# Kernel tuning notes

Hardware: AMD Instinct MI355X
Metric: run time of the kernel (lower is better)

## Reference

```python
import jax, jax.numpy as jnp
import numpy as np

BOUND = 10.0
EPS = 1e-06
MIN_SCALE = 1e-4


def _params_to_spline(raw_w, raw_h, raw_s, bound):
    # Standard Durkan et al. rational-quadratic spline parameterization.
    # raw_w/raw_h: (1, D, K); raw_s: (1, D, K+1)
    two_b = 2.0 * bound
    widths = jax.nn.softmax(raw_w[0], axis=-1) * two_b      # (D, K)
    heights = jax.nn.softmax(raw_h[0], axis=-1) * two_b     # (D, K)
    zero = jnp.zeros(widths.shape[:-1] + (1,), widths.dtype)
    xk = -bound + jnp.concatenate([zero, jnp.cumsum(widths, axis=-1)], axis=-1)   # (D, K+1)
    yk = -bound + jnp.concatenate([zero, jnp.cumsum(heights, axis=-1)], axis=-1)  # (D, K+1)
    slopes = jax.nn.softplus(raw_s[0])                       # (D, K+1)
    return xk, yk, widths, heights, slopes


def _rqs_forward(z, xk, yk, widths, heights, slopes, bound):
    # z: (B, D); per-dim knots xk/yk: (D, K+1); widths/heights: (D, K); slopes: (D, K+1)
    B, D = z.shape
    K = widths.shape[-1]
    zc = jnp.clip(z, -bound, bound)
    # per-dim binary search over knot positions
    idx = jax.vmap(lambda knots, col: jnp.searchsorted(knots, col, side='right'),
                   in_axes=(0, 1), out_axes=1)(xk, zc) - 1
    idx = jnp.clip(idx, 0, K - 1)                            # (B, D)
    di = jnp.arange(D)[None, :]
    xk_sel = xk[di, idx]
    w_sel = widths[di, idx]
    yk_sel = yk[di, idx]
    h_sel = heights[di, idx]
    d0 = slopes[di, idx]
    d1 = slopes[di, idx + 1]
    theta = (zc - xk_sel) / w_sel
    s = h_sel / w_sel
    t1m = theta * (1.0 - theta)
    den = s + (d0 + d1 - 2.0 * s) * t1m
    y_in = yk_sel + h_sel * (s * theta * theta + d0 * t1m) / den
    inside = (z > -bound) & (z < bound)
    return jnp.where(inside, y_in, z)


def setup_inputs() -> dict:
    key = jax.random.key(0)
    ks = jax.random.split(key, 7)
    B, D, K = 8192, 1024, 64
    return {
        'u': jax.random.uniform(ks[0], (B, D), dtype=jnp.float32),
        'tau': jax.random.normal(ks[1], (B, 1), dtype=jnp.float32),
        'log_scale': jax.random.normal(ks[2], (D,), dtype=jnp.float32) * 0.1,
        'bias': jax.random.normal(ks[3], (D,), dtype=jnp.float32) * 0.1,
        'raw_w': jax.random.normal(ks[4], (1, D, K), dtype=jnp.float32) * 0.5,
        'raw_h': jax.random.normal(ks[5], (1, D, K), dtype=jnp.float32) * 0.5,
        'raw_s': jax.random.normal(ks[6], (1, D, K + 1), dtype=jnp.float32) * 0.5,
    }


def reference(u, tau, log_scale, bias, raw_w, raw_h, raw_s):
    # logit input transform
    u_safe = jnp.clip(u, EPS, 1.0 - EPS)
    z = jnp.log(u_safe) - jnp.log1p(-u_safe)
    xk, yk, widths, heights, slopes = _params_to_spline(raw_w, raw_h, raw_s, BOUND)
    z = _rqs_forward(z, xk, yk, widths, heights, slopes, BOUND)
    scale = jax.nn.softplus(log_scale) + MIN_SCALE
    q = z * scale[None, :] + bias[None, :]
    return tau * q  # tau (B,1) broadcasts to (B,D)
```

## Files before the change

### kernel.cpp

```cpp
#include <hip/hip_runtime.h>
#include <math.h>

#define BOUNDF 10.0f
#define EPSF 1e-6f
#define MIN_SCALEF 1e-4f
#define DD 1024
#define KK 64
#define KP1 65

#define TD 64
#define TR 128

__global__ __launch_bounds__(64) void rqs_precompute(
    const float* __restrict__ raw_w, const float* __restrict__ raw_h,
    const float* __restrict__ raw_s, const float* __restrict__ log_scale,
    float* __restrict__ xk, float* __restrict__ yk,
    float* __restrict__ sl, float* __restrict__ scale)
{
    const int d = blockIdx.x;
    const int k = threadIdx.x;

    float ew = __expf(raw_w[d * KK + k]);
    float eh = __expf(raw_h[d * KK + k]);

    float sw = ew, sh = eh;
#pragma unroll
    for (int off = 1; off < 64; off <<= 1) {
        sw += __shfl_xor(sw, off, 64);
        sh += __shfl_xor(sh, off, 64);
    }
    float wk = ew * (2.0f * BOUNDF) / sw;
    float hk = eh * (2.0f * BOUNDF) / sh;

    float cw = wk, ch = hk;
#pragma unroll
    for (int off = 1; off < 64; off <<= 1) {
        float tw = __shfl_up(cw, off, 64);
        float th = __shfl_up(ch, off, 64);
        if (k >= off) { cw += tw; ch += th; }
    }
    xk[d * KP1 + k + 1] = -BOUNDF + cw;
    yk[d * KP1 + k + 1] = -BOUNDF + ch;

    float rs = raw_s[d * KP1 + k];
    sl[d * KP1 + k] = log1pf(__expf(rs));
    if (k == 0) {
        xk[d * KP1] = -BOUNDF;
        yk[d * KP1] = -BOUNDF;
        float rs2 = raw_s[d * KP1 + KK];
        sl[d * KP1 + KK] = log1pf(__expf(rs2));
        scale[d] = log1pf(__expf(log_scale[d])) + MIN_SCALEF;
    }
}

__global__ __launch_bounds__(256) void rqs_main(
    const float* __restrict__ u, const float* __restrict__ tau,
    const float* __restrict__ bias,
    const float* __restrict__ xk_g, const float* __restrict__ yk_g,
    const float* __restrict__ sl_g, const float* __restrict__ scale_g,
    float* __restrict__ out)
{
    __shared__ float lxk[TD * KP1];
    __shared__ float lyk[TD * KP1];
    __shared__ float lsl[TD * KP1];

    const int bx = blockIdx.x;
    const int dchunk = bx & (DD / TD - 1);
    const int rchunk = bx >> 4;
    const int d0 = dchunk * TD;
    const int r0 = rchunk * TR;
    const int t = threadIdx.x;

    for (int i = t; i < TD * KP1; i += 256) {
        lxk[i] = xk_g[d0 * KP1 + i];
        lyk[i] = yk_g[d0 * KP1 + i];
        lsl[i] = sl_g[d0 * KP1 + i];
    }
    __syncthreads();

    const int g = t & 15;
    const int rlane = t >> 4;
    const int dl = g * 4;
    const int dg = d0 + dl;

    float sc[4], bi[4];
#pragma unroll
    for (int j = 0; j < 4; ++j) {
        sc[j] = scale_g[dg + j];
        bi[j] = bias[dg + j];
    }

#pragma unroll 1
    for (int it = 0; it < TR / 16; ++it) {
        const int b = r0 + it * 16 + rlane;
        const float4 uu = *(const float4*)(u + (size_t)b * DD + dg);
        const float tb = tau[b];
        float ua[4] = {uu.x, uu.y, uu.z, uu.w};
        float res[4];
#pragma unroll
        for (int j = 0; j < 4; ++j) {
            float uv = fminf(fmaxf(ua[j], EPSF), 1.0f - EPSF);
            float z = __logf(uv) - __logf(1.0f - uv);
            float zc = fminf(fmaxf(z, -BOUNDF), BOUNDF);
            const int base = (dl + j) * KP1;
            int lo = 0;
#pragma unroll
            for (int s = 32; s >= 1; s >>= 1) {
                lo += (lxk[base + lo + s] <= zc) ? s : 0;
            }
            float x0 = lxk[base + lo], x1 = lxk[base + lo + 1];
            float y0 = lyk[base + lo], y1 = lyk[base + lo + 1];
            float s0 = lsl[base + lo], s1 = lsl[base + lo + 1];
            float w = x1 - x0, h = y1 - y0;
            float invw = __builtin_amdgcn_rcpf(w);
            float th = (zc - x0) * invw;
            float sm = h * invw;
            float t1m = th * (1.0f - th);
            float den = fmaf(fmaf(-2.0f, sm, s0 + s1), t1m, sm);
            float num = h * fmaf(sm * th, th, s0 * t1m);
            float y = fmaf(num, __builtin_amdgcn_rcpf(den), y0);
            y = (z > -BOUNDF && z < BOUNDF) ? y : z;
            res[j] = tb * fmaf(y, sc[j], bi[j]);
        }
        float4 ro = make_float4(res[0], res[1], res[2], res[3]);
        *(float4*)(out + (size_t)b * DD + dg) = ro;
    }
}

extern "C" void kernel_launch(void* const* d_in, const int* in_sizes, int n_in,
                              void* d_out, int out_size, void* d_ws, size_t ws_size,
                              hipStream_t stream)
{
    const float* u         = (const float*)d_in[0];
    const float* tau       = (const float*)d_in[1];
    const float* log_scale = (const float*)d_in[2];
    const float* bias      = (const float*)d_in[3];
    const float* raw_w     = (const float*)d_in[4];
    const float* raw_h     = (const float*)d_in[5];
    const float* raw_s     = (const float*)d_in[6];
    float* out = (float*)d_out;

    float* ws    = (float*)d_ws;
    float* xk    = ws;
    float* yk    = xk + DD * KP1;
    float* sl    = yk + DD * KP1;
    float* scale = sl + DD * KP1;

    const int B = in_sizes[0] / DD;

    rqs_precompute<<<DD, 64, 0, stream>>>(raw_w, raw_h, raw_s, log_scale,
                                          xk, yk, sl, scale);
    rqs_main<<<(DD / TD) * (B / TR), 256, 0, stream>>>(u, tau, bias,
                                                       xk, yk, sl, scale, out);
}
```

Measured before the change: 116.8 us.

## Halve D-tile, cache upper search knots in registers, prefetch next row

Shrinks the per-block D tile from 64 to 32, which halves the shared memory used for knot tables and allows more resident blocks; launch bounds now request 6 blocks. The first three levels of the per-element binary search now read from seven knot values held in registers instead of shared memory. The next row's u and tau are loaded before computing the current row, and the logit uses one log plus a reciprocal instead of two logs. In exchange, knot tables are reloaded from global memory by twice as many blocks, and the extra registers may pressure occupancy.

```diff
diff --git a/kernel.cpp b/kernel.cpp
--- a/kernel.cpp
+++ b/kernel.cpp
@@ -8,7 +8,7 @@
 #define KK 64
 #define KP1 65
 
-#define TD 64
+#define TD 32
 #define TR 128
 
 __global__ __launch_bounds__(64) void rqs_precompute(
@@ -53,7 +53,7 @@
     }
 }
 
-__global__ __launch_bounds__(256) void rqs_main(
+__global__ __launch_bounds__(256, 6) void rqs_main(
     const float* __restrict__ u, const float* __restrict__ tau,
     const float* __restrict__ bias,
     const float* __restrict__ xk_g, const float* __restrict__ yk_g,
@@ -66,7 +66,7 @@
 
     const int bx = blockIdx.x;
     const int dchunk = bx & (DD / TD - 1);
-    const int rchunk = bx >> 4;
+    const int rchunk = bx >> 5;
     const int d0 = dchunk * TD;
     const int r0 = rchunk * TR;
     const int t = threadIdx.x;
@@ -78,36 +78,55 @@
     }
     __syncthreads();
 
-    const int g = t & 15;
-    const int rlane = t >> 4;
+    const int g = t & 7;
+    const int rlane = t >> 3;
     const int dl = g * 4;
     const int dg = d0 + dl;
 
     float sc[4], bi[4];
+    float kreg[4][7];
 #pragma unroll
     for (int j = 0; j < 4; ++j) {
         sc[j] = scale_g[dg + j];
         bi[j] = bias[dg + j];
+        const int base = (dl + j) * KP1;
+#pragma unroll
+        for (int i = 0; i < 7; ++i) kreg[j][i] = lxk[base + 8 * (i + 1)];
     }
 
+    int b = r0 + rlane;
+    float4 uu = *(const float4*)(u + (size_t)b * DD + dg);
+    float tb = tau[b];
+
 #pragma unroll 1
-    for (int it = 0; it < TR / 16; ++it) {
-        const int b = r0 + it * 16 + rlane;
-        const float4 uu = *(const float4*)(u + (size_t)b * DD + dg);
-        const float tb = tau[b];
-        float ua[4] = {uu.x, uu.y, uu.z, uu.w};
+    for (int it = 0; it < TR / 32; ++it) {
+        const int bcur = b;
+        const float4 ucur = uu;
+        const float tcur = tb;
+        if (it + 1 < TR / 32) {
+            const int bn = bcur + 32;
+            uu = *(const float4*)(u + (size_t)bn * DD + dg);
+            tb = tau[bn];
+            b = bn;
+        }
+        float ua[4] = {ucur.x, ucur.y, ucur.z, ucur.w};
         float res[4];
 #pragma unroll
         for (int j = 0; j < 4; ++j) {
             float uv = fminf(fmaxf(ua[j], EPSF), 1.0f - EPSF);
-            float z = __logf(uv) - __logf(1.0f - uv);
+            float z = __logf(uv * __builtin_amdgcn_rcpf(1.0f - uv));
             float zc = fminf(fmaxf(z, -BOUNDF), BOUNDF);
             const int base = (dl + j) * KP1;
-            int lo = 0;
-#pragma unroll
-            for (int s = 32; s >= 1; s >>= 1) {
-                lo += (lxk[base + lo + s] <= zc) ? s : 0;
-            }
+            int lo = (zc >= kreg[j][3]) ? 32 : 0;
+            float m16 = (lo & 32) ? kreg[j][5] : kreg[j][1];
+            lo += (zc >= m16) ? 16 : 0;
+            float a8 = (lo & 32) ? kreg[j][4] : kreg[j][0];
+            float b8 = (lo & 32) ? kreg[j][6] : kreg[j][2];
+            float m8 = (lo & 16) ? b8 : a8;
+            lo += (zc >= m8) ? 8 : 0;
+            lo += (lxk[base + lo + 4] <= zc) ? 4 : 0;
+            lo += (lxk[base + lo + 2] <= zc) ? 2 : 0;
+            lo += (lxk[base + lo + 1] <= zc) ? 1 : 0;
             float x0 = lxk[base + lo], x1 = lxk[base + lo + 1];
             float y0 = lyk[base + lo], y1 = lyk[base + lo + 1];
             float s0 = lsl[base + lo], s1 = lsl[base + lo + 1];
@@ -120,10 +139,10 @@
             float num = h * fmaf(sm * th, th, s0 * t1m);
             float y = fmaf(num, __builtin_amdgcn_rcpf(den), y0);
             y = (z > -BOUNDF && z < BOUNDF) ? y : z;
-            res[j] = tb * fmaf(y, sc[j], bi[j]);
+            res[j] = tcur * fmaf(y, sc[j], bi[j]);
         }
         float4 ro = make_float4(res[0], res[1], res[2], res[3]);
-        *(float4*)(out + (size_t)b * DD + dg) = ro;
+        *(float4*)(out + (size_t)bcur * DD + dg) = ro;
     }
 }
 
```

Result: faster. 111.0 us (-5.0%).

## Map one thread per dimension and track search bounds in registers

Applied to the files above, without the earlier changes.

Shrinks the dimension tile from 64 to 32 and gives each thread a single dimension with scalar loads instead of float4 over four dimensions. This spreads shared-memory knot lookups across banks and avoids the strided-bank conflicts of the old mapping. The binary search now carries the bracketing knot values in registers, removing two shared loads, and the logit is computed with one log and a reciprocal. Softplus in the precompute kernel uses fast log. Costs are narrower 4-byte global accesses, more blocks each reloading the knot tables, and slightly lower precision in the logit and softplus.

```diff
diff --git a/kernel.cpp b/kernel.cpp
--- a/kernel.cpp
+++ b/kernel.cpp
@@ -8,7 +8,7 @@
 #define KK 64
 #define KP1 65
 
-#define TD 64
+#define TD 32
 #define TR 128
 
 __global__ __launch_bounds__(64) void rqs_precompute(
@@ -43,13 +43,13 @@
     yk[d * KP1 + k + 1] = -BOUNDF + ch;
 
     float rs = raw_s[d * KP1 + k];
-    sl[d * KP1 + k] = log1pf(__expf(rs));
+    sl[d * KP1 + k] = __logf(1.0f + __expf(rs));
     if (k == 0) {
         xk[d * KP1] = -BOUNDF;
         yk[d * KP1] = -BOUNDF;
         float rs2 = raw_s[d * KP1 + KK];
-        sl[d * KP1 + KK] = log1pf(__expf(rs2));
-        scale[d] = log1pf(__expf(log_scale[d])) + MIN_SCALEF;
+        sl[d * KP1 + KK] = __logf(1.0f + __expf(rs2));
+        scale[d] = __logf(1.0f + __expf(log_scale[d])) + MIN_SCALEF;
     }
 }
 
@@ -66,7 +66,7 @@
 
     const int bx = blockIdx.x;
     const int dchunk = bx & (DD / TD - 1);
-    const int rchunk = bx >> 4;
+    const int rchunk = bx >> 5;
     const int d0 = dchunk * TD;
     const int r0 = rchunk * TR;
     const int t = threadIdx.x;
@@ -78,52 +78,48 @@
     }
     __syncthreads();
 
-    const int g = t & 15;
-    const int rlane = t >> 4;
-    const int dl = g * 4;
-    const int dg = d0 + dl;
+    const int dim = t & (TD - 1);
+    const int rbase = t >> 5;
+    const int d = d0 + dim;
+    const int base = dim * KP1;
 
-    float sc[4], bi[4];
+    const float sc = scale_g[d];
+    const float bi = bias[d];
+
+#pragma unroll 2
+    for (int it = 0; it < TR / 8; ++it) {
+        const int row = r0 + it * 8 + rbase;
+        const float uval = u[(size_t)row * DD + d];
+        const float tb = tau[row];
+
+        float uv = fminf(fmaxf(uval, EPSF), 1.0f - EPSF);
+        float z = __logf(uv * __builtin_amdgcn_rcpf(1.0f - uv));
+        float zc = fminf(fmaxf(z, -BOUNDF), BOUNDF);
+
+        int lo = 0;
+        float xlo = -BOUNDF, xhi = BOUNDF;
 #pragma unroll
-    for (int j = 0; j < 4; ++j) {
-        sc[j] = scale_g[dg + j];
-        bi[j] = bias[dg + j];
-    }
+        for (int s = 32; s >= 1; s >>= 1) {
+            float m = lxk[base + lo + s];
+            bool c = (m <= zc);
+            lo += c ? s : 0;
+            xlo = c ? m : xlo;
+            xhi = c ? xhi : m;
+        }
 
-#pragma unroll 1
-    for (int it = 0; it < TR / 16; ++it) {
-        const int b = r0 + it * 16 + rlane;
-        const float4 uu = *(const float4*)(u + (size_t)b * DD + dg);
-        const float tb = tau[b];
-        float ua[4] = {uu.x, uu.y, uu.z, uu.w};
-        float res[4];
-#pragma unroll
-        for (int j = 0; j < 4; ++j) {
-            float uv = fminf(fmaxf(ua[j], EPSF), 1.0f - EPSF);
-            float z = __logf(uv) - __logf(1.0f - uv);
-            float zc = fminf(fmaxf(z, -BOUNDF), BOUNDF);
-            const int base = (dl + j) * KP1;
-            int lo = 0;
-#pragma unroll
-            for (int s = 32; s >= 1; s >>= 1) {
-                lo += (lxk[base + lo + s] <= zc) ? s : 0;
-            }
-            float x0 = lxk[base + lo], x1 = lxk[base + lo + 1];
-            float y0 = lyk[base + lo], y1 = lyk[base + lo + 1];
-            float s0 = lsl[base + lo], s1 = lsl[base + lo + 1];
-            float w = x1 - x0, h = y1 - y0;
-            float invw = __builtin_amdgcn_rcpf(w);
-            float th = (zc - x0) * invw;
-            float sm = h * invw;
-            float t1m = th * (1.0f - th);
-            float den = fmaf(fmaf(-2.0f, sm, s0 + s1), t1m, sm);
-            float num = h * fmaf(sm * th, th, s0 * t1m);
-            float y = fmaf(num, __builtin_amdgcn_rcpf(den), y0);
-            y = (z > -BOUNDF && z < BOUNDF) ? y : z;
-            res[j] = tb * fmaf(y, sc[j], bi[j]);
-        }
-        float4 ro = make_float4(res[0], res[1], res[2], res[3]);
-        *(float4*)(out + (size_t)b * DD + dg) = ro;
+        float y0 = lyk[base + lo], y1 = lyk[base + lo + 1];
+        float s0 = lsl[base + lo], s1 = lsl[base + lo + 1];
+        float w = xhi - xlo, h = y1 - y0;
+        float invw = __builtin_amdgcn_rcpf(w);
+        float th = (zc - xlo) * invw;
+        float sm = h * invw;
+        float t1m = th * (1.0f - th);
+        float den = fmaf(fmaf(-2.0f, sm, s0 + s1), t1m, sm);
+        float num = h * fmaf(sm * th, th, s0 * t1m);
+        float y = fmaf(num, __builtin_amdgcn_rcpf(den), y0);
+        y = (z > -BOUNDF && z < BOUNDF) ? y : z;
+
+        out[(size_t)row * DD + d] = tb * fmaf(y, sc, bi);
     }
 }
 
```

After: 112.7 us. -3.5%, faster.
